# Kernel optimization log

Measured on AMD Instinct MI355X. Metric: run time of the kernel, lower is better.

Reference implementation:

```python
import jax, jax.numpy as jnp
import numpy as np

N_DIV = 8

def setup_inputs() -> dict:
    key = jax.random.key(0)
    k1, k2, k3 = jax.random.split(key, 3)
    x = jax.random.normal(k1, (8, 128, 8, 56, 56), dtype=jnp.float32)
    conv_weight = jax.random.normal(k2, (3,), dtype=jnp.float32)
    conv_bias = jax.random.normal(k3, (1,), dtype=jnp.float32)
    return {"x": x, "conv_weight": conv_weight, "conv_bias": conv_bias}

def reference(x, conv_weight, conv_bias):
    # x: (B, C, T, H, W) with T == n_div == 8
    B, C, T, H, W = x.shape
    # view (B*C, n_div, H, W); zero-pad the n_div axis by 1 on each side
    xg = x.reshape(B * C, N_DIV, H, W)
    xp = jnp.pad(xg, ((0, 0), (1, 1), (0, 0), (0, 0)))
    # 1x1 Conv2d(3->1) over sliding window of 3 along padded axis ==
    # 3-tap weighted sum + bias, fully vectorized (no python loop over data dims)
    w0, w1, w2 = conv_weight[0], conv_weight[1], conv_weight[2]
    fused = (w0 * xp[:, :-2] + w1 * xp[:, 1:-1] + w2 * xp[:, 2:]) + conv_bias[0]
    # (B*C, n_div, H, W) -> (B, C, n_div, H, W) -> (B, n_div, C, H, W) -> (B*T, C, H, W)
    out = fused.reshape(B, C, N_DIV, H, W).transpose(0, 2, 1, 3, 4)
    return out.reshape(B * T, C, H, W)
```

## Files before the change

kernel.cpp:

```cpp
#include <hip/hip_runtime.h>


typedef float f32x4 __attribute__((ext_vector_type(4)));

#define B_   8
#define C_   128
#define T_   8
#define HW4  784
#define TOT4 (B_ * T_ * C_ * HW4)
#define UNROLL 4
#define NTH  (TOT4 / UNROLL)
#define GRID (NTH / 256)

__global__ __launch_bounds__(256) void temporal_interaction_kernel(
    const f32x4* __restrict__ in4,
    const float* __restrict__ cw,
    const float* __restrict__ cb,
    f32x4* __restrict__ out4)
{
    const float w1 = cw[1];
    const float bs = cb[0];

    const int i0 = blockIdx.x * 256 + threadIdx.x;

    int hw = i0 % HW4;
    int r  = i0 / HW4;
    int c  = r % C_;
    int r2 = r / C_;
    int t  = r2 % T_;
    int b0 = r2 / T_;

    const float wp = (t > 0)      ? cw[0] : 0.f;
    const float wn = (t < T_ - 1) ? cw[2] : 0.f;
    const int   dp = (t > 0)      ? -HW4 : 0;
    const int   dn = (t < T_ - 1) ?  HW4 : 0;

    int base = ((b0 * C_ + c) * T_ + t) * HW4 + hw;

    #pragma unroll
    for (int k = 0; k < UNROLL; ++k) {
        const int ib = base + k * NTH;
        const int io = i0   + k * NTH;

        f32x4 ctr = in4[ib];
        f32x4 prv = in4[ib + dp];
        f32x4 nxt = in4[ib + dn];

        f32x4 o;
        o.x = fmaf(wp, prv.x, fmaf(w1, ctr.x, fmaf(wn, nxt.x, bs)));
        o.y = fmaf(wp, prv.y, fmaf(w1, ctr.y, fmaf(wn, nxt.y, bs)));
        o.z = fmaf(wp, prv.z, fmaf(w1, ctr.z, fmaf(wn, nxt.z, bs)));
        o.w = fmaf(wp, prv.w, fmaf(w1, ctr.w, fmaf(wn, nxt.w, bs)));

        __builtin_nontemporal_store(o, &out4[io]);
    }
}

extern "C" void kernel_launch(void* const* d_in, const int* in_sizes, int n_in,
                              void* d_out, int out_size, void* d_ws, size_t ws_size,
                              hipStream_t stream) {
    const f32x4* in4 = (const f32x4*)d_in[0];
    const float* cw  = (const float*)d_in[1];
    const float* cb  = (const float*)d_in[2];
    f32x4* out4 = (f32x4*)d_out;

    temporal_interaction_kernel<<<GRID, 256, 0, stream>>>(in4, cw, cb, out4);
}
```

Before: 37.16 us.

## Load all eight temporal slices per thread and reuse them in registers

Each thread now loads the full T=8 column for one (b,c,hw4) position into registers and computes all eight outputs from it. This replaces three loads per output, which relied on cache hits for the neighbour slices, with one load per element. It cuts the grid by a factor of two and raises register use, which may reduce memory-level parallelism per thread.

Result: faster. 34.88 us (-6.1%).

```diff
diff --git a/kernel.cpp b/kernel.cpp
--- a/kernel.cpp
+++ b/kernel.cpp
@@ -7,9 +7,7 @@
 #define C_   128
 #define T_   8
 #define HW4  784
-#define TOT4 (B_ * T_ * C_ * HW4)
-#define UNROLL 4
-#define NTH  (TOT4 / UNROLL)
+#define NTH  (B_ * C_ * HW4)
 #define GRID (NTH / 256)
 
 __global__ __launch_bounds__(256) void temporal_interaction_kernel(
@@ -18,41 +16,40 @@
     const float* __restrict__ cb,
     f32x4* __restrict__ out4)
 {
+    const float w0 = cw[0];
     const float w1 = cw[1];
+    const float w2 = cw[2];
     const float bs = cb[0];
 
     const int i0 = blockIdx.x * 256 + threadIdx.x;
+    const int hw = i0 % HW4;
+    const int bc = i0 / HW4;
+    const int b  = bc / C_;
+    const int c  = bc % C_;
 
-    int hw = i0 % HW4;
-    int r  = i0 / HW4;
-    int c  = r % C_;
-    int r2 = r / C_;
-    int t  = r2 % T_;
-    int b0 = r2 / T_;
+    const f32x4* src = in4 + bc * (T_ * HW4) + hw;
 
-    const float wp = (t > 0)      ? cw[0] : 0.f;
-    const float wn = (t < T_ - 1) ? cw[2] : 0.f;
-    const int   dp = (t > 0)      ? -HW4 : 0;
-    const int   dn = (t < T_ - 1) ?  HW4 : 0;
+    f32x4 x[T_];
+    #pragma unroll
+    for (int t = 0; t < T_; ++t) x[t] = src[t * HW4];
 
-    int base = ((b0 * C_ + c) * T_ + t) * HW4 + hw;
+    const int obase = (b * T_ * C_ + c) * HW4 + hw;
 
     #pragma unroll
-    for (int k = 0; k < UNROLL; ++k) {
-        const int ib = base + k * NTH;
-        const int io = i0   + k * NTH;
+    for (int t = 0; t < T_; ++t) {
+        f32x4 o;
+        const float px = (t > 0)      ? 1.f : 0.f;
+        const float nx = (t < T_ - 1) ? 1.f : 0.f;
+        const f32x4 prv = (t > 0)      ? x[t - 1] : (f32x4)(0.f);
+        const f32x4 nxt = (t < T_ - 1) ? x[t + 1] : (f32x4)(0.f);
+        (void)px; (void)nx;
 
-        f32x4 ctr = in4[ib];
-        f32x4 prv = in4[ib + dp];
-        f32x4 nxt = in4[ib + dn];
+        o.x = fmaf(w0, prv.x, fmaf(w1, x[t].x, fmaf(w2, nxt.x, bs)));
+        o.y = fmaf(w0, prv.y, fmaf(w1, x[t].y, fmaf(w2, nxt.y, bs)));
+        o.z = fmaf(w0, prv.z, fmaf(w1, x[t].z, fmaf(w2, nxt.z, bs)));
+        o.w = fmaf(w0, prv.w, fmaf(w1, x[t].w, fmaf(w2, nxt.w, bs)));
 
-        f32x4 o;
-        o.x = fmaf(wp, prv.x, fmaf(w1, ctr.x, fmaf(wn, nxt.x, bs)));
-        o.y = fmaf(wp, prv.y, fmaf(w1, ctr.y, fmaf(wn, nxt.y, bs)));
-        o.z = fmaf(wp, prv.z, fmaf(w1, ctr.z, fmaf(wn, nxt.z, bs)));
-        o.w = fmaf(wp, prv.w, fmaf(w1, ctr.w, fmaf(wn, nxt.w, bs)));
-
-        __builtin_nontemporal_store(o, &out4[io]);
+        __builtin_nontemporal_store(o, &out4[obase + t * (C_ * HW4)]);
     }
 }
 
```
